# Kernel tuning notes

Hardware: AMD Instinct MI355X
Metric: run time of the kernel (lower is better)

The kernel has to match this reference:

```python
import jax, jax.numpy as jnp
import numpy as np
jax.config.update("jax_enable_x64", True)

TAPS, DELAY = 5, 3
EPS = 1e-6        # DNN_WPE.eps: power clamp before WPE
WPE_EPS = 1e-10   # wpe_one_iteration eps: inverse-power clamp + diag loading


def _signal_framing(Y, L):
    # Y: (..., T) -> (..., T-L+1, L) sliding frames (as_strided equivalent)
    T = Y.shape[-1]
    idx = jnp.arange(T - L + 1)[:, None] + jnp.arange(L)[None, :]
    return Y[..., idx]


def _wpe_one_iteration(Y, power, taps, delay):
    # Y: (B,F,C,T) complex128, power: (B,F,T) float64
    B, F, C, T = Y.shape
    inv_power = 1.0 / jnp.maximum(power, WPE_EPS)
    Tp = T - delay - taps + 1
    # tap-stacked delayed signal, taps axis reversed: (B,F,C,Tp,taps)
    Psi = _signal_framing(Y, taps)[..., :Tp, :][..., ::-1]
    Psi_n = Psi.conj() * inv_power[:, :, None, delay + taps - 1:, None]
    # covariance R: (B,F,taps*C,taps*C); cross-corr P: (B,F,taps,C_e,C_d)
    R = jnp.einsum("bfdtk,bfetl->bfkdle", Psi_n, Psi).reshape(B, F, taps * C, taps * C)
    P = jnp.einsum("bfdtk,bfet->bfked", Psi_n, Y[..., delay + taps - 1:])
    # v: (B,F,C_e,taps*C_d); conj filter G = inv(R) @ v^T  (X = v @ inv(R)^T)
    v = P.transpose(0, 1, 3, 2, 4).reshape(B, F, C, taps * C)
    eye = jnp.eye(taps * C, dtype=R.dtype)
    tr = jnp.trace(R, axis1=-2, axis2=-1).real[..., None, None] / (taps * C)
    G = jnp.linalg.solve(R + WPE_EPS * tr * eye, v.transpose(0, 1, 3, 2))
    G = G.reshape(B, F, taps, C, C)  # (B,F,tau,d,e) conjugated filter matrix
    # reverb tail: sum over taps of filtered, delayed signal
    tail = jnp.zeros_like(Y)
    for tau in range(taps):  # taps=5, small fixed loop
        s = delay + tau
        contrib = jnp.einsum("bfde,bfdt->bfet", G[:, :, tau], Y[..., : T - s])
        tail = tail.at[..., s:].add(contrib)
    return Y - tail


def setup_inputs() -> dict:
    key = jax.random.key(0)
    k1, k2, k3 = jax.random.split(key, 3)
    B, T, C, F = 4, 512, 8, 257
    data_real = jax.random.normal(k1, (B, T, C, F), dtype=jnp.float32)
    data_imag = jax.random.normal(k2, (B, T, C, F), dtype=jnp.float32)
    ilens = jax.random.randint(k3, (B,), 256, T + 1)
    return {"data_real": data_real, "data_imag": data_imag, "ilens": ilens}


def reference(data_real, data_imag, ilens):
    # (B,T,C,F) -> (B,F,C,T)
    data = (data_real + 1j * data_imag).transpose(0, 3, 2, 1)
    # power averaged over channels, clamped (B,F,T)
    power = jnp.maximum(jnp.mean(data.real ** 2 + data.imag ** 2, axis=-2), EPS)
    enh = _wpe_one_iteration(data.astype(jnp.complex128), power.astype(jnp.float64), TAPS, DELAY)
    enh = enh.astype(jnp.complex64)
    T = enh.shape[-1]
    pad = (jnp.arange(T)[None, :] >= ilens[:, None])[:, None, None, :]  # (B,1,1,T)
    enh = jnp.where(pad, 0.0 + 0.0j, enh)
    enh = enh.transpose(0, 3, 2, 1)  # back to (B,T,C,F)
    return enh.real, enh.imag, power
```

## Files before the change

kernel.cpp:

```cpp
#include <hip/hip_runtime.h>
#include <hip/hip_fp16.h>

#define B_ 4
#define T_ 512
#define C_ 8
#define F_ 257
#define TAPS 5
#define DELAY 3
#define N_ 40
#define NA 48
#define TP 505
#define T0 7
#define BF (B_*F_)
#define BTCF ((size_t)B_*T_*C_*F_)
#define YSH 532
#define YPAD 8
#define AUGSZ 1180
#define ZSD 36

typedef _Float16 half8 __attribute__((ext_vector_type(8)));
typedef float floatx4 __attribute__((ext_vector_type(4)));
typedef uint32_t uint32x4 __attribute__((ext_vector_type(4)));

__device__ inline uint32_t h2mul(uint32_t a, uint32_t b) {
    __half2 r = __hmul2(__builtin_bit_cast(__half2, a), __builtin_bit_cast(__half2, b));
    return __builtin_bit_cast(uint32_t, r);
}
__device__ inline uint32_t packf16(float2 v) {
    __half2 h = __floats2half2_rn(v.x, v.y);
    return __builtin_bit_cast(uint32_t, h);
}
__device__ inline float2 unpackf16(uint32_t u) {
    __half2 h = __builtin_bit_cast(__half2, u);
    return make_float2(__low2float(h), __high2float(h));
}
__device__ inline half8 mkfrag(uint32_t a, uint32_t b, uint32_t c, uint32_t d) {
    uint32x4 v = {a, b, c, d};
    return __builtin_bit_cast(half8, v);
}
__device__ inline int rowoff(int i) {
    return i * 49 - ((i * (i - 1)) >> 1);
}

struct Frag { half8 X; half8 Y; };

__device__ inline Frag build2(const uint32_t* p, uint32_t sw0, uint32_t sw1,
                              uint32_t sw2, uint32_t sw3) {
    uint32_t q0 = p[0], q1 = p[1], q2 = p[2], q3 = p[3];
    uint32_t q4 = p[4], q5 = p[5], q6 = p[6], q7 = p[7];
    uint32_t x0 = __builtin_amdgcn_perm(q1, q0, 0x05040100);
    uint32_t y0 = __builtin_amdgcn_perm(q1, q0, 0x07060302);
    uint32_t x1 = __builtin_amdgcn_perm(q3, q2, 0x05040100);
    uint32_t y1 = __builtin_amdgcn_perm(q3, q2, 0x07060302);
    uint32_t x2 = __builtin_amdgcn_perm(q5, q4, 0x05040100);
    uint32_t y2 = __builtin_amdgcn_perm(q5, q4, 0x07060302);
    uint32_t x3 = __builtin_amdgcn_perm(q7, q6, 0x05040100);
    uint32_t y3 = __builtin_amdgcn_perm(q7, q6, 0x07060302);
    Frag f;
    f.X = mkfrag(h2mul(x0, sw0), h2mul(x1, sw1), h2mul(x2, sw2), h2mul(x3, sw3));
    f.Y = mkfrag(h2mul(y0, sw0), h2mul(y1, sw1), h2mul(y2, sw2), h2mul(y3, sw3));
    return f;
}
__device__ inline int zs_off(int j) {
    return (j < N_) ? (j & 7) * YSH + (YPAD + 4 - (j >> 3)) : (j - N_) * YSH + (YPAD + T0);
}

__global__ __launch_bounds__(256) void k_fused(const float* __restrict__ in_re,
                                               const float* __restrict__ in_im,
                                               const int* __restrict__ ilens,
                                               float* __restrict__ out_re,
                                               float* __restrict__ out_im,
                                               float* __restrict__ pow_out) {
    __shared__ uint32_t sYh[C_ * YSH];
    __shared__ __align__(16) float uScr[640];
    __shared__ __align__(16) uint32_t sw_pk[256];
    __shared__ __align__(16) float2 sAugU[AUGSZ];
    float* sPow = uScr;
    float2* sGT = (float2*)uScr;
    int tid = threadIdx.x;

    int bid = blockIdx.x;
    int xcd = bid & 7, slot = bid >> 3;
    int w = (xcd < 4) ? xcd * 129 + slot : 516 + (xcd - 4) * 128 + slot;
    int b = w / F_;
    int f = w - b * F_;
    int ilen = ilens[b];
    const float* pre = in_re + (size_t)b * T_ * C_ * F_ + f;
    const float* pim = in_im + (size_t)b * T_ * C_ * F_ + f;

    {
        int t0 = tid, t1 = tid + 256;
        float s0 = 0.f, s1 = 0.f;
#pragma unroll 4
        for (int c = 0; c < C_; ++c) {
            size_t a0 = ((size_t)t0 * C_ + c) * F_;
            size_t a1 = ((size_t)t1 * C_ + c) * F_;
            float xr0 = pre[a0], xi0 = pim[a0];
            float xr1 = pre[a1], xi1 = pim[a1];
            sYh[c * YSH + YPAD + t0] = packf16(make_float2(xr0, xi0));
            sYh[c * YSH + YPAD + t1] = packf16(make_float2(xr1, xi1));
            s0 += xr0 * xr0 + xi0 * xi0;
            s1 += xr1 * xr1 + xi1 * xi1;
        }
        if (tid < 20) {
            int z = (tid < 8) ? tid : (512 + tid);
#pragma unroll
            for (int c = 0; c < C_; ++c) sYh[c * YSH + z] = 0;
        }
        s0 = fmaxf(s0 * (1.0f / C_), 1e-6f);
        s1 = fmaxf(s1 * (1.0f / C_), 1e-6f);
        pow_out[(size_t)w * T_ + t0] = s0;
        pow_out[(size_t)w * T_ + t1] = s1;
        sPow[t0] = s0;
        sPow[t1] = s1;
    }
    __syncthreads();

    {
        int k0 = 2 * tid, k1 = k0 + 1;
        float w0 = (k0 < TP) ? rsqrtf(sPow[k0 + T0]) : 0.f;
        float w1 = (k1 < TP) ? rsqrtf(sPow[k1 + T0]) : 0.f;
        sw_pk[tid] = packf16(make_float2(w0, w1));
    }
    __syncthreads();

    int wv = tid >> 6, ln = tid & 63;
    int kg = ln >> 4;
    if (wv < 3) {
        int r16 = ln & 15;
        int offB = zs_off(wv * 16 + r16);
#pragma unroll 1
        for (int mt = 0; mt < 3; ++mt) {
            int offA = zs_off(mt * 16 + r16);
            floatx4 aRe = {0.f, 0.f, 0.f, 0.f};
            floatx4 aIm = {0.f, 0.f, 0.f, 0.f};
#pragma unroll 2
            for (int ks = 0; ks < 16; ++ks) {
                int kbase = ks * 32 + kg * 8;
                uint32x4 sv = *(const uint32x4*)&sw_pk[kbase >> 1];
                Frag B = build2(&sYh[offB + kbase], sv[0], sv[1], sv[2], sv[3]);
                Frag A = build2(&sYh[offA + kbase], sv[0], sv[1], sv[2], sv[3]);
                half8 nYa = -A.Y;
                aRe = __builtin_amdgcn_mfma_f32_16x16x32_f16(A.X, B.X, aRe, 0, 0, 0);
                aRe = __builtin_amdgcn_mfma_f32_16x16x32_f16(A.Y, B.Y, aRe, 0, 0, 0);
                aIm = __builtin_amdgcn_mfma_f32_16x16x32_f16(A.X, B.Y, aIm, 0, 0, 0);
                aIm = __builtin_amdgcn_mfma_f32_16x16x32_f16(nYa, B.X, aIm, 0, 0, 0);
            }
#pragma unroll
            for (int r = 0; r < 4; ++r) {
                int m = mt * 16 + kg * 4 + r;
                int col = wv * 16 + r16;
                if (m < N_ && col >= m)
                    sAugU[rowoff(m) + col - m] = make_float2(aRe[r], aIm[r]);
            }
        }
    }
    __syncthreads();

    if (tid < 64) {
        float dv = (tid < N_) ? sAugU[rowoff(tid)].x : 0.f;
#pragma unroll
        for (int off = 32; off; off >>= 1) dv += __shfl_xor(dv, off, 64);
        if (tid < N_) sAugU[rowoff(tid)].x += 1e-10f * dv / N_;
    }
    __syncthreads();

    {
        int ri = tid >> 4, ci = tid & 15;
#pragma unroll 1
        for (int p = 0; p < N_ - 1; ++p) {
            int rop = rowoff(p);
            float2 piv = sAugU[rop];
            float dnm = piv.x * piv.x + piv.y * piv.y;
            float pix = piv.x / dnm, piy = -piv.y / dnm;
#pragma unroll 1
            for (int i = p + 1 + ri; i < N_; i += 16) {
                float2 api = sAugU[rop + i - p];
                float mx = api.x * pix + api.y * piy;
                float my = api.x * piy - api.y * pix;
                int roi = rowoff(i) - i;
#pragma unroll 1
                for (int j = i + ci; j < NA; j += 16) {
                    float2 apj = sAugU[rop + j - p];
                    float2 v = sAugU[roi + j];
                    v.x -= mx * apj.x - my * apj.y;
                    v.y -= mx * apj.y + my * apj.x;
                    sAugU[roi + j] = v;
                }
            }
            __syncthreads();
        }
    }
    {
        int bc = tid & 7, br = tid >> 3;
#pragma unroll 1
        for (int p = N_ - 1; p > 0; --p) {
            int rop = rowoff(p);
            float2 piv = sAugU[rop];
            float dnm = piv.x * piv.x + piv.y * piv.y;
            float pix = piv.x / dnm, piy = -piv.y / dnm;
            float2 rhs = sAugU[rop + N_ + bc - p];
            float xr = rhs.x * pix - rhs.y * piy;
            float xi = rhs.x * piy + rhs.y * pix;
#pragma unroll 1
            for (int i = br; i < p; i += 32) {
                int roi = rowoff(i) - i;
                float2 aip = sAugU[roi + p];
                float2 v = sAugU[roi + N_ + bc];
                v.x -= aip.x * xr - aip.y * xi;
                v.y -= aip.x * xi + aip.y * xr;
                sAugU[roi + N_ + bc] = v;
            }
            __syncthreads();
        }
    }
    for (int idx = tid; idx < N_ * C_; idx += 256) {
        int j = idx >> 3;
        int e = idx & 7;
        int roj = rowoff(j);
        float2 piv = sAugU[roj];
        float dnm = piv.x * piv.x + piv.y * piv.y;
        float pix = piv.x / dnm, piy = -piv.y / dnm;
        float2 rhs = sAugU[roj + N_ + e - j];
        int tau = j >> 3, d = j & 7;
        sGT[(e * C_ + d) * TAPS + tau] =
            make_float2(rhs.x * pix - rhs.y * piy, rhs.x * piy + rhs.y * pix);
    }
    __syncthreads();

    uint32_t* zBuf = (uint32_t*)sAugU;
    half8 aFr[2], aFi[2];
    {
        int m = ln & 15;
#pragma unroll
        for (int ks = 0; ks < 2; ++ks) {
            half8 hr = {}, hi = {};
#pragma unroll
            for (int q = 0; q < 8; ++q) {
                int j = ks * 32 + kg * 8 + q;
                float gx = 0.f, gy = 0.f;
                if (m < 8 && j < N_) {
                    float2 g = sGT[(m * C_ + (j & 7)) * TAPS + (j >> 3)];
                    gx = g.x; gy = g.y;
                }
                hr[q] = (_Float16)gx;
                hi[q] = (_Float16)gy;
            }
            aFr[ks] = hr;
            aFi[ks] = hi;
        }
    }
    for (int idx = tid; idx < 64 * ZSD; idx += 256) zBuf[idx] = 0;
    __syncthreads();

    int trow = wv * 16 + (ln & 15);
#pragma unroll 1
    for (int ch = 0; ch < 8; ++ch) {
        int c0 = ch * 64;
        for (int idx = tid; idx < 1280; idx += 256) {
            int jp = idx >> 6, tl = idx & 63;
            int j0 = 2 * jp, j1 = j0 + 1;
            int base = c0 + tl + (YPAD - 3);
            uint32_t y0 = sYh[(j0 & 7) * YSH + base - (j0 >> 3)];
            uint32_t y1 = sYh[(j1 & 7) * YSH + base - (j1 >> 3)];
            zBuf[tl * ZSD + jp] = __builtin_amdgcn_perm(y1, y0, 0x05040100);
        }
        __syncthreads();
        floatx4 accR = {0.f, 0.f, 0.f, 0.f};
        floatx4 accI = {0.f, 0.f, 0.f, 0.f};
#pragma unroll
        for (int ks = 0; ks < 2; ++ks) {
            int o = trow * ZSD + ks * 16 + kg * 4;
            half8 Br = __builtin_bit_cast(half8, *(const uint32x4*)&zBuf[o]);
            accR = __builtin_amdgcn_mfma_f32_16x16x32_f16(aFr[ks], Br, accR, 0, 0, 0);
            accI = __builtin_amdgcn_mfma_f32_16x16x32_f16(aFi[ks], Br, accI, 0, 0, 0);
        }
        __syncthreads();
        for (int idx = tid; idx < 1280; idx += 256) {
            int jp = idx >> 6, tl = idx & 63;
            int j0 = 2 * jp, j1 = j0 + 1;
            int base = c0 + tl + (YPAD - 3);
            uint32_t y0 = sYh[(j0 & 7) * YSH + base - (j0 >> 3)];
            uint32_t y1 = sYh[(j1 & 7) * YSH + base - (j1 >> 3)];
            zBuf[tl * ZSD + jp] = __builtin_amdgcn_perm(y1, y0, 0x07060302);
        }
        __syncthreads();
#pragma unroll
        for (int ks = 0; ks < 2; ++ks) {
            int o = trow * ZSD + ks * 16 + kg * 4;
            half8 Bi = __builtin_bit_cast(half8, *(const uint32x4*)&zBuf[o]);
            half8 nFi = -aFi[ks];
            accR = __builtin_amdgcn_mfma_f32_16x16x32_f16(nFi, Bi, accR, 0, 0, 0);
            accI = __builtin_amdgcn_mfma_f32_16x16x32_f16(aFr[ks], Bi, accI, 0, 0, 0);
        }
        if (kg < 2) {
            int tg = c0 + trow;
            bool dead = (tg >= ilen);
#pragma unroll
            for (int r = 0; r < 4; ++r) {
                int e = kg * 4 + r;
                float2 cf = unpackf16(sYh[e * YSH + YPAD + tg]);
                float ex = cf.x - accR[r];
                float ey = cf.y - accI[r];
                if (dead) { ex = 0.f; ey = 0.f; }
                size_t o = (size_t)b * T_ * C_ * F_ + ((size_t)tg * C_ + e) * F_ + f;
                out_re[o] = ex;
                out_im[o] = ey;
            }
        }
        __syncthreads();
    }
}

extern "C" void kernel_launch(void* const* d_in, const int* in_sizes, int n_in,
                              void* d_out, int out_size, void* d_ws, size_t ws_size,
                              hipStream_t stream) {
    const float* in_re = (const float*)d_in[0];
    const float* in_im = (const float*)d_in[1];
    const int* ilens = (const int*)d_in[2];

    float* out_re = (float*)d_out;
    float* out_im = out_re + BTCF;
    float* out_pw = out_im + BTCF;

    k_fused<<<BF, 256, 0, stream>>>(in_re, in_im, ilens, out_re, out_im, out_pw);
}
```

Baseline: 189.4 us.

## Block LU elimination two pivots per step and merge real/imag Z staging

Gaussian elimination and back substitution now handle two pivots per barrier-separated step, roughly halving the number of __syncthreads in the 40x40 complex solve. The pivot-row update is deferred and written at the start of the next step. The MFMA tail stage builds separate real and imaginary Z buffers in one pass from a pooled shared-memory region, which removes two barriers per chunk and the zero-fill. The cost is more arithmetic per step and more complex indexing, with some risk to numerical robustness.

After: 188.3 us. No clear change (-0.6%).

```diff
diff --git a/kernel.cpp b/kernel.cpp
--- a/kernel.cpp
+++ b/kernel.cpp
@@ -15,8 +15,7 @@
 #define BTCF ((size_t)B_*T_*C_*F_)
 #define YSH 532
 #define YPAD 8
-#define AUGSZ 1180
-#define ZSD 36
+#define ZSD 20
 
 typedef _Float16 half8 __attribute__((ext_vector_type(8)));
 typedef float floatx4 __attribute__((ext_vector_type(4)));
@@ -72,11 +71,11 @@
                                                float* __restrict__ out_im,
                                                float* __restrict__ pow_out) {
     __shared__ uint32_t sYh[C_ * YSH];
-    __shared__ __align__(16) float uScr[640];
-    __shared__ __align__(16) uint32_t sw_pk[256];
-    __shared__ __align__(16) float2 sAugU[AUGSZ];
-    float* sPow = uScr;
-    float2* sGT = (float2*)uScr;
+    __shared__ __align__(16) uint32_t pool[3256];
+    float* sPow = (float*)pool;
+    float2* sGT = (float2*)pool;
+    uint32_t* sw_pk = pool + 640;
+    float2* sAugU = (float2*)(pool + 896);
     int tid = threadIdx.x;
 
     int bid = blockIdx.x;
@@ -167,17 +166,85 @@
 
     {
         int ri = tid >> 4, ci = tid & 15;
-#pragma unroll 1
-        for (int p = 0; p < N_ - 1; ++p) {
+        float2 dq0, dq1, dq2;
+#pragma unroll 1
+        for (int p = 0; p < N_ - 2; p += 2) {
+            if (p > 0 && ri == 0) {
+                int qm = p - 1, roqm = rowoff(qm);
+                if (ci < NA - qm)      sAugU[roqm + ci] = dq0;
+                if (ci + 16 < NA - qm) sAugU[roqm + ci + 16] = dq1;
+                if (ci + 32 < NA - qm) sAugU[roqm + ci + 32] = dq2;
+            }
+            int q = p + 1;
+            int rop = rowoff(p), roq = rowoff(q);
+            float2 Upp = sAugU[rop];
+            float2 Upq = sAugU[rop + 1];
+            float2 Uqq = sAugU[roq];
+            float dn0 = Upp.x * Upp.x + Upp.y * Upp.y;
+            float i0x = Upp.x / dn0, i0y = -Upp.y / dn0;
+            float mqx = Upq.x * i0x + Upq.y * i0y;
+            float mqy = Upq.x * i0y - Upq.y * i0x;
+            float d1x = Uqq.x - (mqx * Upq.x - mqy * Upq.y);
+            float d1y = Uqq.y - (mqx * Upq.y + mqy * Upq.x);
+            float dn1 = d1x * d1x + d1y * d1y;
+            float i1x = d1x / dn1, i1y = -d1y / dn1;
+#pragma unroll 1
+            for (int i = q + ri; i < N_; i += 16) {
+                if (i == q) {
+#pragma unroll
+                    for (int s = 0; s < 3; ++s) {
+                        int j = q + ci + 16 * s;
+                        float2 r = make_float2(0.f, 0.f);
+                        if (j < NA) {
+                            float2 Upj = sAugU[rop + j - p];
+                            float2 Uqj = sAugU[roq + j - q];
+                            r.x = Uqj.x - (mqx * Upj.x - mqy * Upj.y);
+                            r.y = Uqj.y - (mqx * Upj.y + mqy * Upj.x);
+                        }
+                        if (s == 0) dq0 = r; else if (s == 1) dq1 = r; else dq2 = r;
+                    }
+                } else {
+                    float2 Upi = sAugU[rop + i - p];
+                    float m0x = Upi.x * i0x + Upi.y * i0y;
+                    float m0y = Upi.x * i0y - Upi.y * i0x;
+                    float2 Uqi = sAugU[roq + i - q];
+                    float ax = Uqi.x - (m0x * Upq.x - m0y * Upq.y);
+                    float ay = -Uqi.y - (m0x * Upq.y + m0y * Upq.x);
+                    float m1x = ax * i1x - ay * i1y;
+                    float m1y = ax * i1y + ay * i1x;
+                    int roi = rowoff(i) - i;
+#pragma unroll 1
+                    for (int j = i + ci; j < NA; j += 16) {
+                        float2 Upj = sAugU[rop + j - p];
+                        float2 Uqj = sAugU[roq + j - q];
+                        float u1x = Uqj.x - (mqx * Upj.x - mqy * Upj.y);
+                        float u1y = Uqj.y - (mqx * Upj.y + mqy * Upj.x);
+                        float2 v = sAugU[roi + j];
+                        v.x -= (m0x * Upj.x - m0y * Upj.y) + (m1x * u1x - m1y * u1y);
+                        v.y -= (m0x * Upj.y + m0y * Upj.x) + (m1x * u1y + m1y * u1x);
+                        sAugU[roi + j] = v;
+                    }
+                }
+            }
+            __syncthreads();
+        }
+        {
+            int p = N_ - 2;
+            if (ri == 0) {
+                int qm = p - 1, roqm = rowoff(qm);
+                if (ci < NA - qm)      sAugU[roqm + ci] = dq0;
+                if (ci + 16 < NA - qm) sAugU[roqm + ci + 16] = dq1;
+                if (ci + 32 < NA - qm) sAugU[roqm + ci + 32] = dq2;
+            }
             int rop = rowoff(p);
             float2 piv = sAugU[rop];
-            float dnm = piv.x * piv.x + piv.y * piv.y;
-            float pix = piv.x / dnm, piy = -piv.y / dnm;
+            float dn = piv.x * piv.x + piv.y * piv.y;
+            float px = piv.x / dn, py = -piv.y / dn;
 #pragma unroll 1
             for (int i = p + 1 + ri; i < N_; i += 16) {
                 float2 api = sAugU[rop + i - p];
-                float mx = api.x * pix + api.y * piy;
-                float my = api.x * piy - api.y * pix;
+                float mx = api.x * px + api.y * py;
+                float my = api.x * py - api.y * px;
                 int roi = rowoff(i) - i;
 #pragma unroll 1
                 for (int j = i + ci; j < NA; j += 16) {
@@ -193,23 +260,59 @@
     }
     {
         int bc = tid & 7, br = tid >> 3;
-#pragma unroll 1
-        for (int p = N_ - 1; p > 0; --p) {
-            int rop = rowoff(p);
+        float2 defv = make_float2(0.f, 0.f);
+        int defRow = -1;
+#pragma unroll 1
+        for (int p = N_ - 1; p >= 3; p -= 2) {
+            if (defRow >= 0 && br == (defRow & 31))
+                sAugU[rowoff(defRow) + N_ + bc - defRow] = defv;
+            int q = p - 1;
+            int rop = rowoff(p), roq = rowoff(q);
+            float2 pivP = sAugU[rop];
+            float dnP = pivP.x * pivP.x + pivP.y * pivP.y;
+            float pPx = pivP.x / dnP, pPy = -pivP.y / dnP;
+            float2 rhsP = sAugU[rop + N_ + bc - p];
+            float xPx = rhsP.x * pPx - rhsP.y * pPy;
+            float xPy = rhsP.x * pPy + rhsP.y * pPx;
+            float2 pivQ = sAugU[roq];
+            float dnQ = pivQ.x * pivQ.x + pivQ.y * pivQ.y;
+            float pQx = pivQ.x / dnQ, pQy = -pivQ.y / dnQ;
+            float2 Uqp = sAugU[roq + 1];
+            float2 rhsQ = sAugU[roq + N_ + bc - q];
+            float rqx = rhsQ.x - (Uqp.x * xPx - Uqp.y * xPy);
+            float rqy = rhsQ.y - (Uqp.x * xPy + Uqp.y * xPx);
+            float xQx = rqx * pQx - rqy * pQy;
+            float xQy = rqx * pQy + rqy * pQx;
+#pragma unroll 1
+            for (int i = br; i <= p - 2; i += 32) {
+                int roi = rowoff(i) - i;
+                float2 Uip = sAugU[roi + p];
+                float2 Uiq = sAugU[roi + q];
+                float2 v = sAugU[roi + N_ + bc];
+                v.x -= (Uip.x * xPx - Uip.y * xPy) + (Uiq.x * xQx - Uiq.y * xQy);
+                v.y -= (Uip.x * xPy + Uip.y * xPx) + (Uiq.x * xQy + Uiq.y * xQx);
+                sAugU[roi + N_ + bc] = v;
+            }
+            if (br == (q & 31)) defv = make_float2(rqx, rqy);
+            defRow = q;
+            __syncthreads();
+        }
+        {
+            if (defRow >= 0 && br == (defRow & 31))
+                sAugU[rowoff(defRow) + N_ + bc - defRow] = defv;
+            int rop = rowoff(1);
             float2 piv = sAugU[rop];
-            float dnm = piv.x * piv.x + piv.y * piv.y;
-            float pix = piv.x / dnm, piy = -piv.y / dnm;
-            float2 rhs = sAugU[rop + N_ + bc - p];
-            float xr = rhs.x * pix - rhs.y * piy;
-            float xi = rhs.x * piy + rhs.y * pix;
-#pragma unroll 1
-            for (int i = br; i < p; i += 32) {
-                int roi = rowoff(i) - i;
-                float2 aip = sAugU[roi + p];
-                float2 v = sAugU[roi + N_ + bc];
+            float dn = piv.x * piv.x + piv.y * piv.y;
+            float px = piv.x / dn, py = -piv.y / dn;
+            float2 rhs = sAugU[rop + N_ + bc - 1];
+            float xr = rhs.x * px - rhs.y * py;
+            float xi = rhs.x * py + rhs.y * px;
+            if (br == 0) {
+                float2 aip = sAugU[1];
+                float2 v = sAugU[N_ + bc];
                 v.x -= aip.x * xr - aip.y * xi;
                 v.y -= aip.x * xi + aip.y * xr;
-                sAugU[roi + N_ + bc] = v;
+                sAugU[N_ + bc] = v;
             }
             __syncthreads();
         }
@@ -228,7 +331,6 @@
     }
     __syncthreads();
 
-    uint32_t* zBuf = (uint32_t*)sAugU;
     half8 aFr[2], aFi[2];
     {
         int m = ln & 15;
@@ -250,9 +352,10 @@
             aFi[ks] = hi;
         }
     }
-    for (int idx = tid; idx < 64 * ZSD; idx += 256) zBuf[idx] = 0;
-    __syncthreads();
-
+    __syncthreads();
+
+    uint32_t* zRe = pool;
+    uint32_t* zIm = pool + 64 * ZSD;
     int trow = wv * 16 + (ln & 15);
 #pragma unroll 1
     for (int ch = 0; ch < 8; ++ch) {
@@ -263,35 +366,31 @@
             int base = c0 + tl + (YPAD - 3);
             uint32_t y0 = sYh[(j0 & 7) * YSH + base - (j0 >> 3)];
             uint32_t y1 = sYh[(j1 & 7) * YSH + base - (j1 >> 3)];
-            zBuf[tl * ZSD + jp] = __builtin_amdgcn_perm(y1, y0, 0x05040100);
+            zRe[tl * ZSD + jp] = __builtin_amdgcn_perm(y1, y0, 0x05040100);
+            zIm[tl * ZSD + jp] = __builtin_amdgcn_perm(y1, y0, 0x07060302);
         }
         __syncthreads();
         floatx4 accR = {0.f, 0.f, 0.f, 0.f};
         floatx4 accI = {0.f, 0.f, 0.f, 0.f};
-#pragma unroll
-        for (int ks = 0; ks < 2; ++ks) {
-            int o = trow * ZSD + ks * 16 + kg * 4;
-            half8 Br = __builtin_bit_cast(half8, *(const uint32x4*)&zBuf[o]);
-            accR = __builtin_amdgcn_mfma_f32_16x16x32_f16(aFr[ks], Br, accR, 0, 0, 0);
-            accI = __builtin_amdgcn_mfma_f32_16x16x32_f16(aFi[ks], Br, accI, 0, 0, 0);
-        }
-        __syncthreads();
-        for (int idx = tid; idx < 1280; idx += 256) {
-            int jp = idx >> 6, tl = idx & 63;
-            int j0 = 2 * jp, j1 = j0 + 1;
-            int base = c0 + tl + (YPAD - 3);
-            uint32_t y0 = sYh[(j0 & 7) * YSH + base - (j0 >> 3)];
-            uint32_t y1 = sYh[(j1 & 7) * YSH + base - (j1 >> 3)];
-            zBuf[tl * ZSD + jp] = __builtin_amdgcn_perm(y1, y0, 0x07060302);
-        }
-        __syncthreads();
-#pragma unroll
-        for (int ks = 0; ks < 2; ++ks) {
-            int o = trow * ZSD + ks * 16 + kg * 4;
-            half8 Bi = __builtin_bit_cast(half8, *(const uint32x4*)&zBuf[o]);
-            half8 nFi = -aFi[ks];
-            accR = __builtin_amdgcn_mfma_f32_16x16x32_f16(nFi, Bi, accR, 0, 0, 0);
-            accI = __builtin_amdgcn_mfma_f32_16x16x32_f16(aFr[ks], Bi, accI, 0, 0, 0);
+        {
+            int o0 = trow * ZSD + kg * 4;
+            half8 Br0 = __builtin_bit_cast(half8, *(const uint32x4*)&zRe[o0]);
+            half8 Bi0 = __builtin_bit_cast(half8, *(const uint32x4*)&zIm[o0]);
+            half8 Br1 = {}, Bi1 = {};
+            if (kg == 0) {
+                int o1 = trow * ZSD + 16;
+                Br1 = __builtin_bit_cast(half8, *(const uint32x4*)&zRe[o1]);
+                Bi1 = __builtin_bit_cast(half8, *(const uint32x4*)&zIm[o1]);
+            }
+            half8 nFi0 = -aFi[0], nFi1 = -aFi[1];
+            accR = __builtin_amdgcn_mfma_f32_16x16x32_f16(aFr[0], Br0, accR, 0, 0, 0);
+            accR = __builtin_amdgcn_mfma_f32_16x16x32_f16(aFr[1], Br1, accR, 0, 0, 0);
+            accI = __builtin_amdgcn_mfma_f32_16x16x32_f16(aFi[0], Br0, accI, 0, 0, 0);
+            accI = __builtin_amdgcn_mfma_f32_16x16x32_f16(aFi[1], Br1, accI, 0, 0, 0);
+            accR = __builtin_amdgcn_mfma_f32_16x16x32_f16(nFi0, Bi0, accR, 0, 0, 0);
+            accR = __builtin_amdgcn_mfma_f32_16x16x32_f16(nFi1, Bi1, accR, 0, 0, 0);
+            accI = __builtin_amdgcn_mfma_f32_16x16x32_f16(aFr[0], Bi0, accI, 0, 0, 0);
+            accI = __builtin_amdgcn_mfma_f32_16x16x32_f16(aFr[1], Bi1, accI, 0, 0, 0);
         }
         if (kg < 2) {
             int tg = c0 + trow;
```
